# Kernel optimization log

Measured on AMD Instinct MI355X. Metric: run time of the kernel, lower is better.

The kernel has to match this reference:

```python
import jax, jax.numpy as jnp
import numpy as np

VOCAB, EMB, HID, B, T = 32000, 256, 256, 64, 2048


def setup_inputs() -> dict:
    key = jax.random.key(0)
    ks = jax.random.split(key, 6)
    s = 1.0 / np.sqrt(HID)
    return {
        "source": jax.random.randint(ks[0], (B, T), 0, VOCAB),
        "embedding": jax.random.normal(ks[1], (VOCAB, EMB), dtype=jnp.float32) * 0.02,
        "W_ih": jax.random.uniform(ks[2], (EMB, HID), jnp.float32, -s, s),
        "W_hh": jax.random.uniform(ks[3], (HID, HID), jnp.float32, -s, s),
        "b_ih": jax.random.uniform(ks[4], (HID,), jnp.float32, -s, s),
        "b_hh": jax.random.uniform(ks[5], (HID,), jnp.float32, -s, s),
    }


def reference(source, embedding, W_ih, W_hh, b_ih, b_hh):
    # embedding lookup: [B, T, EMB]
    embedded = embedding[source]
    # scan over time with carried hidden state (RNNCellManual: tanh cell)
    xs = jnp.swapaxes(embedded, 0, 1)  # [T, B, EMB]

    def step(h, x_t):
        h_new = jnp.tanh(x_t @ W_ih + b_ih + h @ W_hh + b_hh)
        return h_new, None

    h0 = jnp.zeros((source.shape[0], W_hh.shape[0]), dtype=embedding.dtype)
    h_T, _ = jax.lax.scan(step, h0, xs)
    return h_T  # final hidden state [B, HID]
```

## Files before the change

### kernel.cpp

```cpp
#include <hip/hip_runtime.h>

#define TT 2048
#define BB 64
#define HH 256

typedef _Float16 half2_t __attribute__((ext_vector_type(2)));
typedef _Float16 half8_t __attribute__((ext_vector_type(8)));
typedef float f32x4 __attribute__((ext_vector_type(4)));

__global__ void prep_kernel(const float* __restrict__ Wih, const float* __restrict__ Whh,
                            _Float16* __restrict__ WihT, _Float16* __restrict__ WhhT) {
  const int n = blockIdx.x;
  const int k = threadIdx.x;
  WihT[n * HH + k] = (_Float16)Wih[k * HH + n];
  WhhT[n * HH + k] = (_Float16)Whh[k * HH + n];
}

__global__ __launch_bounds__(256, 2) void embed_gemm_kernel(
    const int* __restrict__ source, const float* __restrict__ emb,
    const _Float16* __restrict__ WihT, const float* __restrict__ b_ih,
    const float* __restrict__ b_hh, _Float16* __restrict__ U) {
  const int t = blockIdx.x;
  const int nbase = blockIdx.y * 64;
  __shared__ __align__(16) _Float16 Bs[64][280];

  const int tid = threadIdx.x;
  for (int c = tid; c < 64 * 32; c += 256) {
    const int n = c >> 5;
    const int ko = (c & 31) * 8;
    *(half8_t*)&Bs[n][ko] = *(const half8_t*)(WihT + (size_t)(nbase + n) * HH + ko);
  }
  __syncthreads();

  const int lane = tid & 63;
  const int wave = tid >> 6;
  const int row16 = lane & 15;
  const int quad = lane >> 4;
  const int b = wave * 16 + row16;
  const int src = source[b * TT + t];
  const float* arow = emb + (size_t)src * HH + quad * 8;

  f32x4 acc[4];
#pragma unroll
  for (int ct = 0; ct < 4; ++ct) acc[ct] = (f32x4){0.f, 0.f, 0.f, 0.f};

#pragma unroll
  for (int kt = 0; kt < 8; ++kt) {
    const float4 x0 = *(const float4*)(arow + kt * 32);
    const float4 x1 = *(const float4*)(arow + kt * 32 + 4);
    half8_t af;
    af[0] = (_Float16)x0.x; af[1] = (_Float16)x0.y;
    af[2] = (_Float16)x0.z; af[3] = (_Float16)x0.w;
    af[4] = (_Float16)x1.x; af[5] = (_Float16)x1.y;
    af[6] = (_Float16)x1.z; af[7] = (_Float16)x1.w;
#pragma unroll
    for (int ct = 0; ct < 4; ++ct) {
      const half8_t bf = *(const half8_t*)&Bs[ct * 16 + row16][quad * 8 + kt * 32];
      acc[ct] = __builtin_amdgcn_mfma_f32_16x16x32_f16(af, bf, acc[ct], 0, 0, 0);
    }
  }

#pragma unroll
  for (int ct = 0; ct < 4; ++ct) {
    const int nn = nbase + ct * 16 + row16;
    const float bias = b_ih[nn] + b_hh[nn];
#pragma unroll
    for (int r = 0; r < 4; ++r) {
      const int bb = wave * 16 + quad * 4 + r;
      U[((size_t)t * BB + bb) * HH + nn] = (_Float16)(acc[ct][r] + bias);
    }
  }
}

__global__ __launch_bounds__(256)
__attribute__((amdgpu_waves_per_eu(1, 1)))
void rnn_scan_kernel(
    const _Float16* __restrict__ U, const _Float16* __restrict__ WhhT,
    float* __restrict__ out) {
  const int b = blockIdx.x;
  const int tid = threadIdx.x;
  const int w = tid >> 6;
  const int l = tid & 63;
  const int col = l & 15;
  const int quad = l >> 4;

  __shared__ __align__(16) _Float16 hbuf[2][HH];

  half8_t wb[4][8];
#pragma unroll
  for (int tt = 0; tt < 4; ++tt) {
    const _Float16* base = WhhT + (size_t)(64 * w + 16 * tt + col) * HH + quad * 8;
#pragma unroll
    for (int j = 0; j < 8; ++j) {
      const int c = (2 * w + j) & 7;
      wb[tt][j] = *(const half8_t*)(base + 32 * c);
    }
  }
  asm volatile("" : "+a"(wb[0][0]), "+a"(wb[0][1]), "+a"(wb[0][2]), "+a"(wb[0][3]),
                    "+a"(wb[0][4]), "+a"(wb[0][5]), "+a"(wb[0][6]), "+a"(wb[0][7]),
                    "+a"(wb[1][0]), "+a"(wb[1][1]), "+a"(wb[1][2]), "+a"(wb[1][3]),
                    "+a"(wb[1][4]), "+a"(wb[1][5]), "+a"(wb[1][6]), "+a"(wb[1][7]));
  asm volatile("" : "+a"(wb[2][0]), "+a"(wb[2][1]), "+a"(wb[2][2]), "+a"(wb[2][3]),
                    "+a"(wb[2][4]), "+a"(wb[2][5]), "+a"(wb[2][6]), "+a"(wb[2][7]),
                    "+a"(wb[3][0]), "+a"(wb[3][1]), "+a"(wb[3][2]), "+a"(wb[3][3]),
                    "+a"(wb[3][4]), "+a"(wb[3][5]), "+a"(wb[3][6]), "+a"(wb[3][7]));

  const int oO0 = 32 * ((2 * w + 0) & 7) + 8 * quad;
  const int oO1 = 32 * ((2 * w + 1) & 7) + 8 * quad;
  const int oX2 = 32 * ((2 * w + 2) & 7) + 8 * quad;
  const int oX3 = 32 * ((2 * w + 3) & 7) + 8 * quad;
  const int oX4 = 32 * ((2 * w + 4) & 7) + 8 * quad;
  const int oX5 = 32 * ((2 * w + 5) & 7) + 8 * quad;
  const int oX6 = 32 * ((2 * w + 6) & 7) + 8 * quad;
  const int oX7 = 32 * ((2 * w + 7) & 7) + 8 * quad;

  hbuf[0][tid] = (_Float16)0.f;

  const _Float16* Up = U + b * HH + tid;
  _Float16 uc[8], un[8];
#pragma unroll
  for (int s = 0; s < 8; ++s) uc[s] = Up[(size_t)s * (BB * HH)];

  float hn = 0.f;
  f32x4 cacc[4];
#pragma unroll
  for (int tt = 0; tt < 4; ++tt) cacc[tt] = (f32x4){0.f, 0.f, 0.f, 0.f};

  {
    half8_t hoA = *(const half8_t*)(hbuf[0] + oO0);
    half8_t hoB = *(const half8_t*)(hbuf[0] + oO1);
    asm volatile("" : "+v"(hoA), "+v"(hoB));
#pragma unroll
    for (int tt = 0; tt < 4; ++tt)
      cacc[tt] = __builtin_amdgcn_mfma_f32_16x16x32_f16(hoA, wb[tt][0], cacc[tt], 0, 0, 0);
#pragma unroll
    for (int tt = 0; tt < 4; ++tt)
      cacc[tt] = __builtin_amdgcn_mfma_f32_16x16x32_f16(hoB, wb[tt][1], cacc[tt], 0, 0, 0);
  }

  for (int tc = 0; tc < TT; tc += 8) {
    const int tn = (tc + 8) & (TT - 1);
#pragma unroll
    for (int s = 0; s < 8; ++s) un[s] = Up[(size_t)(tn + s) * (BB * HH)];

#pragma unroll
    for (int s = 0; s < 8; ++s) {
      const int t = tc + s;

      asm volatile("s_waitcnt lgkmcnt(0)\n\ts_barrier" ::: "memory");

      const _Float16* hb = hbuf[t & 1];
      half8_t h2 = *(const half8_t*)(hb + oX2);
      half8_t h3 = *(const half8_t*)(hb + oX3);
      half8_t h4 = *(const half8_t*)(hb + oX4);
      half8_t h5 = *(const half8_t*)(hb + oX5);
      half8_t h6 = *(const half8_t*)(hb + oX6);
      half8_t h7 = *(const half8_t*)(hb + oX7);
      asm volatile("" : "+v"(h2), "+v"(h3), "+v"(h4), "+v"(h5), "+v"(h6), "+v"(h7));

#pragma unroll
      for (int tt = 0; tt < 4; ++tt)
        cacc[tt] = __builtin_amdgcn_mfma_f32_16x16x32_f16(h2, wb[tt][2], cacc[tt], 0, 0, 0);
#pragma unroll
      for (int tt = 0; tt < 4; ++tt)
        cacc[tt] = __builtin_amdgcn_mfma_f32_16x16x32_f16(h3, wb[tt][3], cacc[tt], 0, 0, 0);
#pragma unroll
      for (int tt = 0; tt < 4; ++tt)
        cacc[tt] = __builtin_amdgcn_mfma_f32_16x16x32_f16(h4, wb[tt][4], cacc[tt], 0, 0, 0);
#pragma unroll
      for (int tt = 0; tt < 4; ++tt)
        cacc[tt] = __builtin_amdgcn_mfma_f32_16x16x32_f16(h5, wb[tt][5], cacc[tt], 0, 0, 0);
#pragma unroll
      for (int tt = 0; tt < 4; ++tt)
        cacc[tt] = __builtin_amdgcn_mfma_f32_16x16x32_f16(h6, wb[tt][6], cacc[tt], 0, 0, 0);
#pragma unroll
      for (int tt = 0; tt < 4; ++tt)
        cacc[tt] = __builtin_amdgcn_mfma_f32_16x16x32_f16(h7, wb[tt][7], cacc[tt], 0, 0, 0);

      float y = cacc[0][0];
      y = (quad == 1) ? cacc[1][0] : y;
      y = (quad == 2) ? cacc[2][0] : y;
      y = (quad == 3) ? cacc[3][0] : y;

      const float a = (float)uc[s] + y;
      const float e = __builtin_amdgcn_exp2f(a * 2.885390081777927f);
      hn = 1.f - 2.f * __builtin_amdgcn_rcpf(e + 1.f);

      _Float16* hb1 = (_Float16*)hbuf[(t + 1) & 1];
      hb1[tid] = (_Float16)hn;
      half8_t hoA = *(const half8_t*)(hb1 + oO0);
      half8_t hoB = *(const half8_t*)(hb1 + oO1);
      asm volatile("" : "+v"(hoA), "+v"(hoB));
#pragma unroll
      for (int tt = 0; tt < 4; ++tt) cacc[tt] = (f32x4){0.f, 0.f, 0.f, 0.f};
#pragma unroll
      for (int tt = 0; tt < 4; ++tt)
        cacc[tt] = __builtin_amdgcn_mfma_f32_16x16x32_f16(hoA, wb[tt][0], cacc[tt], 0, 0, 0);
#pragma unroll
      for (int tt = 0; tt < 4; ++tt)
        cacc[tt] = __builtin_amdgcn_mfma_f32_16x16x32_f16(hoB, wb[tt][1], cacc[tt], 0, 0, 0);
    }
#pragma unroll
    for (int s = 0; s < 8; ++s) uc[s] = un[s];
  }
  out[(size_t)b * HH + tid] = hn;
}

extern "C" void kernel_launch(void* const* d_in, const int* in_sizes, int n_in,
                              void* d_out, int out_size, void* d_ws, size_t ws_size,
                              hipStream_t stream) {
  const int*   source = (const int*)d_in[0];
  const float* emb    = (const float*)d_in[1];
  const float* Wih    = (const float*)d_in[2];
  const float* Whh    = (const float*)d_in[3];
  const float* bih    = (const float*)d_in[4];
  const float* bhh    = (const float*)d_in[5];
  float* out = (float*)d_out;

  char* ws = (char*)d_ws;
  _Float16* U    = (_Float16*)ws;
  _Float16* WihT = (_Float16*)(ws + 67108864);
  _Float16* WhhT = (_Float16*)(ws + 67239936);

  prep_kernel<<<dim3(256), dim3(256), 0, stream>>>(Wih, Whh, WihT, WhhT);
  embed_gemm_kernel<<<dim3(TT, 4), dim3(256), 0, stream>>>(source, emb, WihT, bih, bhh, U);
  rnn_scan_kernel<<<dim3(BB), dim3(256), 0, stream>>>(U, WhhT, out);
}
```

Measured before the change: 914.3 us.

## Pre-convert embedding table to fp16 and batch timesteps per GEMM block

Adds a conversion of the whole embedding table to fp16 in the prep kernel and a new embedding GEMM kernel that gathers fp16 rows and processes four timesteps per block, reusing the staged W_ih tile and biases. The aim is to halve gather bandwidth and cut the cost of reloading the weight tile per block. It adds a full-table conversion pass every call, and the path is used only when the workspace is large enough.

```diff
diff --git a/kernel.cpp b/kernel.cpp
--- a/kernel.cpp
+++ b/kernel.cpp
@@ -3,17 +3,96 @@
 #define TT 2048
 #define BB 64
 #define HH 256
+#define TPB 4
 
 typedef _Float16 half2_t __attribute__((ext_vector_type(2)));
 typedef _Float16 half8_t __attribute__((ext_vector_type(8)));
 typedef float f32x4 __attribute__((ext_vector_type(4)));
 
 __global__ void prep_kernel(const float* __restrict__ Wih, const float* __restrict__ Whh,
-                            _Float16* __restrict__ WihT, _Float16* __restrict__ WhhT) {
-  const int n = blockIdx.x;
-  const int k = threadIdx.x;
-  WihT[n * HH + k] = (_Float16)Wih[k * HH + n];
-  WhhT[n * HH + k] = (_Float16)Whh[k * HH + n];
+                            _Float16* __restrict__ WihT, _Float16* __restrict__ WhhT,
+                            const float* __restrict__ emb, _Float16* __restrict__ emb16,
+                            int do_emb) {
+  if (blockIdx.x < 256) {
+    const int n = blockIdx.x;
+    const int k = threadIdx.x;
+    WihT[n * HH + k] = (_Float16)Wih[k * HH + n];
+    WhhT[n * HH + k] = (_Float16)Whh[k * HH + n];
+  }
+  if (do_emb) {
+    const long nchunk = 32000L * HH / 8;
+    for (long i = (long)blockIdx.x * blockDim.x + threadIdx.x; i < nchunk;
+         i += (long)gridDim.x * blockDim.x) {
+      const float4 x0 = *(const float4*)(emb + 8 * i);
+      const float4 x1 = *(const float4*)(emb + 8 * i + 4);
+      half8_t h;
+      h[0] = (_Float16)x0.x; h[1] = (_Float16)x0.y;
+      h[2] = (_Float16)x0.z; h[3] = (_Float16)x0.w;
+      h[4] = (_Float16)x1.x; h[5] = (_Float16)x1.y;
+      h[6] = (_Float16)x1.z; h[7] = (_Float16)x1.w;
+      *(half8_t*)(emb16 + 8 * i) = h;
+    }
+  }
+}
+
+__global__ __launch_bounds__(256, 2) void embed_gemm16_kernel(
+    const int* __restrict__ source, const _Float16* __restrict__ emb16,
+    const _Float16* __restrict__ WihT, const float* __restrict__ b_ih,
+    const float* __restrict__ b_hh, _Float16* __restrict__ U) {
+  const int t0 = blockIdx.x * TPB;
+  const int nbase = blockIdx.y * 64;
+  __shared__ __align__(16) _Float16 Bs[64][280];
+
+  const int tid = threadIdx.x;
+  for (int c = tid; c < 64 * 32; c += 256) {
+    const int n = c >> 5;
+    const int ko = (c & 31) * 8;
+    *(half8_t*)&Bs[n][ko] = *(const half8_t*)(WihT + (size_t)(nbase + n) * HH + ko);
+  }
+  __syncthreads();
+
+  const int lane = tid & 63;
+  const int wave = tid >> 6;
+  const int row16 = lane & 15;
+  const int quad = lane >> 4;
+  const int b = wave * 16 + row16;
+
+  float bias[4];
+#pragma unroll
+  for (int ct = 0; ct < 4; ++ct) {
+    const int nn = nbase + ct * 16 + row16;
+    bias[ct] = b_ih[nn] + b_hh[nn];
+  }
+
+  for (int ts = 0; ts < TPB; ++ts) {
+    const int t = t0 + ts;
+    const int src = source[b * TT + t];
+    const _Float16* arow = emb16 + (size_t)src * HH + quad * 8;
+
+    f32x4 acc[4];
+#pragma unroll
+    for (int ct = 0; ct < 4; ++ct) acc[ct] = (f32x4){0.f, 0.f, 0.f, 0.f};
+
+#pragma unroll
+    for (int kt = 0; kt < 8; ++kt) {
+      const half8_t af = *(const half8_t*)(arow + kt * 32);
+#pragma unroll
+      for (int ct = 0; ct < 4; ++ct) {
+        const half8_t bf = *(const half8_t*)&Bs[ct * 16 + row16][quad * 8 + kt * 32];
+        acc[ct] = __builtin_amdgcn_mfma_f32_16x16x32_f16(af, bf, acc[ct], 0, 0, 0);
+      }
+    }
+
+#pragma unroll
+    for (int ct = 0; ct < 4; ++ct) {
+      const int nn = nbase + ct * 16 + row16;
+#pragma unroll
+      for (int r = 0; r < 4; ++r) {
+        const int bb = wave * 16 + quad * 4 + r;
+        U[((size_t)t * BB + bb) * HH + nn] = (_Float16)(acc[ct][r] + bias[ct]);
+      }
+    }
+  }
 }
 
 __global__ __launch_bounds__(256, 2) void embed_gemm_kernel(
@@ -218,11 +297,18 @@
   float* out = (float*)d_out;
 
   char* ws = (char*)d_ws;
-  _Float16* U    = (_Float16*)ws;
-  _Float16* WihT = (_Float16*)(ws + 67108864);
-  _Float16* WhhT = (_Float16*)(ws + 67239936);
-
-  prep_kernel<<<dim3(256), dim3(256), 0, stream>>>(Wih, Whh, WihT, WhhT);
-  embed_gemm_kernel<<<dim3(TT, 4), dim3(256), 0, stream>>>(source, emb, WihT, bih, bhh, U);
+  _Float16* U     = (_Float16*)ws;
+  _Float16* WihT  = (_Float16*)(ws + 67108864);
+  _Float16* WhhT  = (_Float16*)(ws + 67239936);
+  _Float16* emb16 = (_Float16*)(ws + 67371008);
+  const size_t need16 = 67371008u + 16384000u;
+
+  if (ws_size >= need16) {
+    prep_kernel<<<dim3(2048), dim3(256), 0, stream>>>(Wih, Whh, WihT, WhhT, emb, emb16, 1);
+    embed_gemm16_kernel<<<dim3(TT / TPB, 4), dim3(256), 0, stream>>>(source, emb16, WihT, bih, bhh, U);
+  } else {
+    prep_kernel<<<dim3(256), dim3(256), 0, stream>>>(Wih, Whh, WihT, WhhT, emb, (_Float16*)WihT, 0);
+    embed_gemm_kernel<<<dim3(TT, 4), dim3(256), 0, stream>>>(source, emb, WihT, bih, bhh, U);
+  }
   rnn_scan_kernel<<<dim3(BB), dim3(256), 0, stream>>>(U, WhhT, out);
 }
```

New measurement: 876.1 us (median of 2 runs). -4.2%, faster.
